# Optimization experiments

Hardware: AMD Instinct MI355X
Metric: run time of the kernel (lower is better)

Reference implementation:

```python
import jax, jax.numpy as jnp
import numpy as np

B, H, IN, OUT = 8192, 1024, 4, 4


def setup_inputs() -> dict:
    key = jax.random.key(0)
    ks = jax.random.split(key, 16)
    s = 1.0 / np.sqrt(H)

    def p(k, shape):
        return jax.random.uniform(k, shape, jnp.float32, -s, s)

    return {
        "context": jax.random.normal(ks[0], (B, H), jnp.float32),
        "wc": p(ks[1], (H // 2, H)),
        "bc": p(ks[2], (H // 2,)),
        "gru1_wi": p(ks[3], (3 * H, H // 2)),
        "gru1_wh": p(ks[4], (3 * H, H)),
        "gru1_bi": p(ks[5], (3 * H,)),
        "gru1_bh": p(ks[6], (3 * H,)),
        "gru2_wi": p(ks[7], (3 * H, H // 2)),
        "gru2_wh": p(ks[8], (3 * H, H)),
        "gru2_bi": p(ks[9], (3 * H,)),
        "gru2_bh": p(ks[10], (3 * H,)),
        "fc_in_w": p(ks[11], (IN, H)),
        "fc_in_b": p(ks[12], (IN,)),
        "fc_out_w": p(ks[13], (OUT, H)),
        "fc_out_b": p(ks[14], (OUT,)),
        "future_length": 30,
        "past_length": 60,
    }


def _gru_unroll(ec, h0, wi, wh, bi, bh, length):
    """Run a PyTorch-semantics GRUCell `length` steps with constant input ec.

    Returns all hidden states stacked: [T, B, H].
    """
    # Input-side gates are constant across steps (input is always ec).
    gi = ec @ wi.T + bi                     # [B, 3H]
    i_r, i_z, i_n = jnp.split(gi, 3, axis=-1)

    def step(h, _):
        gh = h @ wh.T + bh                  # [B, 3H]
        h_r, h_z, h_n = jnp.split(gh, 3, axis=-1)
        r = jax.nn.sigmoid(i_r + h_r)
        z = jax.nn.sigmoid(i_z + h_z)
        n = jnp.tanh(i_n + r * h_n)
        h_new = (1.0 - z) * n + z * h
        return h_new, h_new

    _, hs = jax.lax.scan(step, h0, None, length=length)
    return hs  # [T, B, H]


def reference(context, wc, bc,
              gru1_wi, gru1_wh, gru1_bi, gru1_bh,
              gru2_wi, gru2_wh, gru2_bi, gru2_bh,
              fc_in_w, fc_in_b, fc_out_w, fc_out_b,
              future_length, past_length):
    # encoded_context = relu(context_encoder(context))
    ec = jax.nn.relu(context @ wc.T + bc)   # [B, H/2]

    # Training-mode past-reconstruction branch (decoder1 + fc_in).
    hs1 = _gru_unroll(ec, context, gru1_wi, gru1_wh, gru1_bi, gru1_bh, past_length)
    decoded_inputs = jnp.einsum('tbh,ih->bti', hs1, fc_in_w) + fc_in_b  # [B, T_past, IN]

    # Future-prediction branch (decoder2 + relu + fc_out).
    hs2 = _gru_unroll(ec, context, gru2_wi, gru2_wh, gru2_bi, gru2_bh, future_length)
    outputs = jnp.einsum('tbh,oh->bto', jax.nn.relu(hs2), fc_out_w) + fc_out_b  # [B, T_fut, OUT]

    return (decoded_inputs, outputs)
```

## Files before the change

kernel.cpp:

```cpp
#include <hip/hip_runtime.h>
#include <math.h>

typedef __bf16 bf16;
typedef __bf16 bf16x8 __attribute__((ext_vector_type(8)));
typedef float f32x4 __attribute__((ext_vector_type(4)));

#define B_DIM 8192
#define H_DIM 1024
#define T_PAST 60
#define T_FUT 30

static __device__ __forceinline__ float sigm(float x) {
  return 1.f / (1.f + __expf(-x));
}
static __device__ __forceinline__ float tanh_fast(float x) {
  float xc = fminf(fmaxf(x, -10.f), 10.f);
  float e = __expf(2.f * xc);
  return (e - 1.f) / (e + 1.f);
}

__global__ void detect_dtype(const unsigned int* __restrict__ words,
                             int* __restrict__ is_bf16) {
  const int lane = threadIdx.x;
  int cnt = 0;
  for (int i = 0; i < 64; i++) {
    const unsigned int w = words[lane + i * 64];
    const int e = (w >> 7) & 0xFF;
    cnt += (e >= 100 && e <= 135) ? 1 : 0;
  }
  for (int off = 32; off > 0; off >>= 1) cnt += __shfl_down(cnt, off);
  if (lane == 0) *is_bf16 = (cnt >= 2048) ? 1 : 0;
}

struct ConvDesc { const void* src; bf16* dst; int n; };
struct ConvPack { ConvDesc d[15]; };

__global__ __launch_bounds__(256) void convert_all(ConvPack p,
                                                   const int* __restrict__ flag,
                                                   float* __restrict__ h0a,
                                                   float* __restrict__ h0b) {
  const int ti = blockIdx.y;
  const ConvDesc d = p.d[ti];
  const int bf = *flag;
  const long stride = (long)gridDim.x * 256 * 8;
  for (long base = ((long)blockIdx.x * 256 + threadIdx.x) * 8; base < d.n;
       base += stride) {
    if (base + 8 <= d.n) {
      float f[8];
      if (bf) {
        const uint4 v = *(const uint4*)((const char*)d.src + base * 2);
        *(uint4*)((char*)d.dst + base * 2) = v;
        if (ti == 0 && h0a) {
          const bf16* bv = (const bf16*)&v;
#pragma unroll
          for (int e = 0; e < 8; e++) f[e] = (float)bv[e];
        }
      } else {
        const float* s = (const float*)d.src + base;
        const float4 v0 = *(const float4*)s;
        const float4 v1 = *(const float4*)(s + 4);
        f[0] = v0.x; f[1] = v0.y; f[2] = v0.z; f[3] = v0.w;
        f[4] = v1.x; f[5] = v1.y; f[6] = v1.z; f[7] = v1.w;
        bf16 o[8];
#pragma unroll
        for (int e = 0; e < 8; e++) o[e] = (bf16)f[e];
        *(uint4*)((char*)d.dst + base * 2) = *(const uint4*)o;
      }
      if (ti == 0 && h0a) {
#pragma unroll
        for (int e = 0; e < 8; e++) { h0a[base + e] = f[e]; h0b[base + e] = f[e]; }
      }
    } else {
      for (long e = base; e < d.n; e++) {
        const float f = bf ? (float)((const bf16*)d.src)[e]
                           : ((const float*)d.src)[e];
        d.dst[e] = (bf16)f;
        if (ti == 0 && h0a) { h0a[e] = f; h0b[e] = f; }
      }
    }
  }
}

template <bool RELU, bool GI_BIAS>
__global__ __launch_bounds__(256, 2) void gemm_bt(
    const bf16* __restrict__ A, const bf16* __restrict__ Bm,
    const bf16* __restrict__ bias1, const bf16* __restrict__ bias2,
    bf16* __restrict__ C, int K, int N)
{
  __shared__ __attribute__((aligned(16))) bf16 As[128 * 32];
  __shared__ __attribute__((aligned(16))) bf16 Bs[128 * 32];
  const int tid = threadIdx.x;
  const int wave = tid >> 6, lane = tid & 63;
  const int quad = lane >> 4, l16 = lane & 15;
  const int m0 = blockIdx.x * 128, n0 = blockIdx.y * 128;
  const int wm = (wave & 1) * 64, wn = (wave >> 1) * 64;
  f32x4 acc[4][4] = {};
  for (int k0 = 0; k0 < K; k0 += 32) {
    bf16x8 va[2], vb[2];
#pragma unroll
    for (int rr = 0; rr < 2; rr++) {
      const int c = rr * 256 + tid;
      va[rr] = *(const bf16x8*)(A + (size_t)(m0 + (c >> 2)) * K + (k0 + (c & 3) * 8));
      vb[rr] = *(const bf16x8*)(Bm + (size_t)(n0 + (c >> 2)) * K + (k0 + (c & 3) * 8));
    }
#pragma unroll
    for (int rr = 0; rr < 2; rr++) {
      const int c = rr * 256 + tid;
      *(bf16x8*)(As + (c >> 2) * 32 + (c & 3) * 8) = va[rr];
      *(bf16x8*)(Bs + (c >> 2) * 32 + (c & 3) * 8) = vb[rr];
    }
    __syncthreads();
    bf16x8 af[4], bv[4];
#pragma unroll
    for (int t = 0; t < 4; t++) {
      af[t] = *(const bf16x8*)(As + ((wm + t * 16 + l16) * 32 + quad * 8));
      bv[t] = *(const bf16x8*)(Bs + ((wn + t * 16 + l16) * 32 + quad * 8));
    }
#pragma unroll
    for (int tm = 0; tm < 4; tm++)
#pragma unroll
      for (int tn = 0; tn < 4; tn++)
        acc[tm][tn] = __builtin_amdgcn_mfma_f32_16x16x32_bf16(af[tm], bv[tn], acc[tm][tn], 0, 0, 0);
    __syncthreads();
  }
#pragma unroll
  for (int tn = 0; tn < 4; tn++) {
    const int col = n0 + wn + tn * 16 + l16;
    float bias = (float)bias1[col];
    if (GI_BIAS) {
      if (col < 2 * H_DIM) bias += (float)bias2[col];
    }
#pragma unroll
    for (int tm = 0; tm < 4; tm++) {
#pragma unroll
      for (int r = 0; r < 4; r++) {
        const int row = m0 + wm + tm * 16 + quad * 4 + r;
        float v = acc[tm][tn][r] + bias;
        if (RELU) v = fmaxf(v, 0.f);
        C[(size_t)row * N + col] = (bf16)v;
      }
    }
  }
}

struct GruArgs {
  const bf16* h_in16; const float* h_in32;
  bf16* h_out16; float* h_out32;
  const bf16* gi;
  const bf16* wh;
  const bf16* bh;
  const bf16* fcw;
  float* proj;
  int projT, t, relu;
};

__global__ __launch_bounds__(256, 2) void gru_step(GruArgs g1, GruArgs g2)
{
  const GruArgs G = (blockIdx.z == 0) ? g1 : g2;
  __shared__ __attribute__((aligned(16))) bf16 As[128 * 32];
  __shared__ __attribute__((aligned(16))) bf16 Bs[192 * 32];
  const int tid = threadIdx.x;
  const int wave = tid >> 6, lane = tid & 63;
  const int quad = lane >> 4, l16 = lane & 15;
  const int m0 = blockIdx.x * 128;
  const int j0 = blockIdx.y * 64;
  f32x4 acc[2][12] = {};
  for (int k0 = 0; k0 < H_DIM; k0 += 32) {
    bf16x8 va[2], vb[3];
#pragma unroll
    for (int rr = 0; rr < 2; rr++) {
      const int c = rr * 256 + tid;
      va[rr] = *(const bf16x8*)(G.h_in16 + (size_t)(m0 + (c >> 2)) * H_DIM + (k0 + (c & 3) * 8));
    }
#pragma unroll
    for (int rr = 0; rr < 3; rr++) {
      const int c = rr * 256 + tid;
      const int p = c >> 2;
      const int grow = (p >> 6) * H_DIM + j0 + (p & 63);
      vb[rr] = *(const bf16x8*)(G.wh + (size_t)grow * H_DIM + (k0 + (c & 3) * 8));
    }
#pragma unroll
    for (int rr = 0; rr < 2; rr++) {
      const int c = rr * 256 + tid;
      *(bf16x8*)(As + (c >> 2) * 32 + (c & 3) * 8) = va[rr];
    }
#pragma unroll
    for (int rr = 0; rr < 3; rr++) {
      const int c = rr * 256 + tid;
      *(bf16x8*)(Bs + (c >> 2) * 32 + (c & 3) * 8) = vb[rr];
    }
    __syncthreads();
    bf16x8 af[2];
#pragma unroll
    for (int tm = 0; tm < 2; tm++)
      af[tm] = *(const bf16x8*)(As + ((wave * 32 + tm * 16 + l16) * 32 + quad * 8));
#pragma unroll
    for (int tn = 0; tn < 12; tn++) {
      bf16x8 bv = *(const bf16x8*)(Bs + ((tn * 16 + l16) * 32 + quad * 8));
      acc[0][tn] = __builtin_amdgcn_mfma_f32_16x16x32_bf16(af[0], bv, acc[0][tn], 0, 0, 0);
      acc[1][tn] = __builtin_amdgcn_mfma_f32_16x16x32_bf16(af[1], bv, acc[1][tn], 0, 0, 0);
    }
    __syncthreads();
  }
  float pp[2][4][4];
#pragma unroll
  for (int tm = 0; tm < 2; tm++)
#pragma unroll
    for (int r = 0; r < 4; r++)
#pragma unroll
      for (int i = 0; i < 4; i++) pp[tm][r][i] = 0.f;

#pragma unroll
  for (int tj = 0; tj < 4; tj++) {
    const int jj = tj * 16 + l16;
    const int j = j0 + jj;
    const float bhn = (float)G.bh[2 * H_DIM + j];
    float fw[4];
#pragma unroll
    for (int i = 0; i < 4; i++) fw[i] = (float)G.fcw[i * H_DIM + j];
#pragma unroll
    for (int tm = 0; tm < 2; tm++) {
#pragma unroll
      for (int r = 0; r < 4; r++) {
        const int row = m0 + wave * 32 + tm * 16 + quad * 4 + r;
        const size_t gb = (size_t)row * (3 * H_DIM) + j;
        const float gr = (float)G.gi[gb];
        const float gz = (float)G.gi[gb + H_DIM];
        const float gn = (float)G.gi[gb + 2 * H_DIM];
        const float hr = acc[tm][tj][r];
        const float hz = acc[tm][tj + 4][r];
        const float hn = acc[tm][tj + 8][r];
        const float rg = sigm(gr + hr);
        const float zg = sigm(gz + hz);
        const float ng = tanh_fast(gn + rg * (hn + bhn));
        const size_t hidx = (size_t)row * H_DIM + j;
        const float hold = G.h_in32 ? G.h_in32[hidx] : (float)G.h_in16[hidx];
        const float hnew = (1.f - zg) * ng + zg * hold;
        if (G.h_out32) G.h_out32[hidx] = hnew;
        G.h_out16[hidx] = (bf16)hnew;
        const float act = G.relu ? fmaxf(hnew, 0.f) : hnew;
#pragma unroll
        for (int i = 0; i < 4; i++) pp[tm][r][i] += fw[i] * act;
      }
    }
  }
#pragma unroll
  for (int tm = 0; tm < 2; tm++)
#pragma unroll
    for (int r = 0; r < 4; r++)
#pragma unroll
      for (int i = 0; i < 4; i++) {
        float v = pp[tm][r][i];
        v += __shfl_xor(v, 1);
        v += __shfl_xor(v, 2);
        v += __shfl_xor(v, 4);
        v += __shfl_xor(v, 8);
        if (l16 == 0) {
          const int row = m0 + wave * 32 + tm * 16 + quad * 4 + r;
          atomicAdd(&G.proj[((size_t)row * G.projT + G.t) * 4 + i], v);
        }
      }
}

__global__ __launch_bounds__(256) void finalize(const float* __restrict__ p1,
                                                const float* __restrict__ p2,
                                                const bf16* __restrict__ fib,
                                                const bf16* __restrict__ fob,
                                                const int* __restrict__ flag,
                                                void* __restrict__ out, int n) {
  const int idx = blockIdx.x * 256 + threadIdx.x;
  if (idx >= n) return;
  const int R1 = B_DIM * T_PAST * 4;
  float v;
  if (idx < R1) {
    v = p1[idx] + (float)fib[idx & 3];
  } else {
    const int k = idx - R1;
    v = p2[k] + (float)fob[k & 3];
  }
  if (*flag) ((bf16*)out)[idx] = (bf16)v;
  else       ((float*)out)[idx] = v;
}

extern "C" void kernel_launch(void* const* d_in, const int* in_sizes, int n_in,
                              void* d_out, int out_size, void* d_ws, size_t ws_size,
                              hipStream_t stream)
{
  (void)n_in;
  char* w = (char*)d_ws;
  auto alloc = [&](size_t bytes) -> void* {
    void* p = (void*)w;
    w += (bytes + 255) & ~(size_t)255;
    return p;
  };
  int* flag = (int*)alloc(256);

  bf16* canon[15];
  for (int i = 0; i < 15; i++) canon[i] = (bf16*)alloc((size_t)in_sizes[i] * 2);
  const bf16* ctx  = canon[0];
  const bf16* wc   = canon[1];
  const bf16* bc   = canon[2];
  const bf16* g1wi = canon[3];
  const bf16* g1wh = canon[4];
  const bf16* g1bi = canon[5];
  const bf16* g1bh = canon[6];
  const bf16* g2wi = canon[7];
  const bf16* g2wh = canon[8];
  const bf16* g2bi = canon[9];
  const bf16* g2bh = canon[10];
  const bf16* fiw  = canon[11];
  const bf16* fib  = canon[12];
  const bf16* fow  = canon[13];
  const bf16* fob  = canon[14];

  bf16* ec   = (bf16*)alloc((size_t)B_DIM * 512 * 2);
  bf16* gi1  = (bf16*)alloc((size_t)B_DIM * 3 * H_DIM * 2);
  bf16* gi2  = (bf16*)alloc((size_t)B_DIM * 3 * H_DIM * 2);
  bf16* h116[2] = {(bf16*)alloc((size_t)B_DIM * H_DIM * 2), (bf16*)alloc((size_t)B_DIM * H_DIM * 2)};
  bf16* h216[2] = {(bf16*)alloc((size_t)B_DIM * H_DIM * 2), (bf16*)alloc((size_t)B_DIM * H_DIM * 2)};
  float* proj1 = (float*)alloc((size_t)B_DIM * T_PAST * 4 * 4);
  float* proj2 = (float*)alloc((size_t)B_DIM * T_FUT * 4 * 4);
  float* h132[2] = {nullptr, nullptr};
  float* h232[2] = {nullptr, nullptr};
  const size_t used = (size_t)(w - (char*)d_ws);
  const size_t fp32_need = (size_t)4 * B_DIM * H_DIM * 4 + 4096;
  const bool fp32h = (ws_size > used) && ((ws_size - used) >= fp32_need);
  if (fp32h) {
    h132[0] = (float*)alloc((size_t)B_DIM * H_DIM * 4);
    h132[1] = (float*)alloc((size_t)B_DIM * H_DIM * 4);
    h232[0] = (float*)alloc((size_t)B_DIM * H_DIM * 4);
    h232[1] = (float*)alloc((size_t)B_DIM * H_DIM * 4);
  }

  detect_dtype<<<1, 64, 0, stream>>>((const unsigned int*)d_in[0], flag);

  hipMemsetAsync(proj1, 0,
                 ((size_t)B_DIM * T_PAST * 4 + (size_t)B_DIM * T_FUT * 4) * 4, stream);

  ConvPack cp;
  for (int i = 0; i < 15; i++) { cp.d[i].src = d_in[i]; cp.d[i].dst = canon[i]; cp.d[i].n = in_sizes[i]; }
  convert_all<<<dim3(4096, 15), 256, 0, stream>>>(cp, flag,
      fp32h ? h132[0] : nullptr, fp32h ? h232[0] : nullptr);

  gemm_bt<true, false><<<dim3(64, 4), 256, 0, stream>>>(ctx, wc, bc, nullptr, ec, H_DIM, 512);
  gemm_bt<false, true><<<dim3(64, 24), 256, 0, stream>>>(ec, g1wi, g1bi, g1bh, gi1, 512, 3 * H_DIM);
  gemm_bt<false, true><<<dim3(64, 24), 256, 0, stream>>>(ec, g2wi, g2bi, g2bh, gi2, 512, 3 * H_DIM);

  for (int t = 0; t < T_PAST; t++) {
    const int si = t & 1, so = (t + 1) & 1;
    GruArgs a1;
    a1.h_in16 = (t == 0) ? ctx : h116[si];
    a1.h_in32 = fp32h ? h132[si] : nullptr;
    a1.h_out16 = h116[so];
    a1.h_out32 = fp32h ? h132[so] : nullptr;
    a1.gi = gi1; a1.wh = g1wh; a1.bh = g1bh; a1.fcw = fiw;
    a1.proj = proj1; a1.projT = T_PAST; a1.t = t; a1.relu = 0;
    if (t < T_FUT) {
      GruArgs a2;
      a2.h_in16 = (t == 0) ? ctx : h216[si];
      a2.h_in32 = fp32h ? h232[si] : nullptr;
      a2.h_out16 = h216[so];
      a2.h_out32 = fp32h ? h232[so] : nullptr;
      a2.gi = gi2; a2.wh = g2wh; a2.bh = g2bh; a2.fcw = fow;
      a2.proj = proj2; a2.projT = T_FUT; a2.t = t; a2.relu = 1;
      gru_step<<<dim3(64, 16, 2), 256, 0, stream>>>(a1, a2);
    } else {
      gru_step<<<dim3(64, 16, 1), 256, 0, stream>>>(a1, a1);
    }
  }

  finalize<<<dim3((out_size + 255) / 256), 256, 0, stream>>>(
      proj1, proj2, fib, fob, flag, d_out, out_size);
}
```

Measured before the change: 10.76 ms.

## Use direct global-to-LDS loads with XOR swizzle and XCD-aware block remap

Replaces the register-staged global loads plus LDS stores in both the GEMM and the GRU step kernels with global_load_lds direct-to-LDS 16-byte transfers. The LDS layout is XOR-swizzled per row so the MFMA fragment reads avoid bank conflicts. The GRU step kernel also remaps block indices so blocks on the same XCD share weight-column slices, aiming for better L2 reuse of Wh. This cuts VGPR pressure and LDS write instructions but relies on the wave-contiguous LDS destination layout matching the swizzled addressing.

```diff
diff --git a/kernel.cpp b/kernel.cpp
--- a/kernel.cpp
+++ b/kernel.cpp
@@ -9,6 +9,12 @@
 #define H_DIM 1024
 #define T_PAST 60
 #define T_FUT 30
+
+static __device__ __forceinline__ void gld_lds16(const void* g, void* l) {
+  __builtin_amdgcn_global_load_lds(
+      (const __attribute__((address_space(1))) void*)g,
+      (__attribute__((address_space(3))) void*)l, 16, 0, 0);
+}
 
 static __device__ __forceinline__ float sigm(float x) {
   return 1.f / (1.f + __expf(-x));
@@ -96,25 +102,23 @@
   const int wm = (wave & 1) * 64, wn = (wave >> 1) * 64;
   f32x4 acc[4][4] = {};
   for (int k0 = 0; k0 < K; k0 += 32) {
-    bf16x8 va[2], vb[2];
 #pragma unroll
     for (int rr = 0; rr < 2; rr++) {
       const int c = rr * 256 + tid;
-      va[rr] = *(const bf16x8*)(A + (size_t)(m0 + (c >> 2)) * K + (k0 + (c & 3) * 8));
-      vb[rr] = *(const bf16x8*)(Bm + (size_t)(n0 + (c >> 2)) * K + (k0 + (c & 3) * 8));
-    }
-#pragma unroll
-    for (int rr = 0; rr < 2; rr++) {
-      const int c = rr * 256 + tid;
-      *(bf16x8*)(As + (c >> 2) * 32 + (c & 3) * 8) = va[rr];
-      *(bf16x8*)(Bs + (c >> 2) * 32 + (c & 3) * 8) = vb[rr];
+      const int cg = (c & 3) ^ ((c >> 3) & 3);
+      gld_lds16(A + (size_t)(m0 + (c >> 2)) * K + (k0 + cg * 8),
+                As + (size_t)(rr * 256 + wave * 64) * 8);
+      gld_lds16(Bm + (size_t)(n0 + (c >> 2)) * K + (k0 + cg * 8),
+                Bs + (size_t)(rr * 256 + wave * 64) * 8);
     }
     __syncthreads();
     bf16x8 af[4], bv[4];
 #pragma unroll
     for (int t = 0; t < 4; t++) {
-      af[t] = *(const bf16x8*)(As + ((wm + t * 16 + l16) * 32 + quad * 8));
-      bv[t] = *(const bf16x8*)(Bs + ((wn + t * 16 + l16) * 32 + quad * 8));
+      const int ra = wm + t * 16 + l16;
+      const int rb = wn + t * 16 + l16;
+      af[t] = *(const bf16x8*)(As + (ra * 32 + (quad ^ ((ra >> 1) & 3)) * 8));
+      bv[t] = *(const bf16x8*)(Bs + (rb * 32 + (quad ^ ((rb >> 1) & 3)) * 8));
     }
 #pragma unroll
     for (int tm = 0; tm < 4; tm++)
@@ -162,41 +166,39 @@
   const int tid = threadIdx.x;
   const int wave = tid >> 6, lane = tid & 63;
   const int quad = lane >> 4, l16 = lane & 15;
-  const int m0 = blockIdx.x * 128;
-  const int j0 = blockIdx.y * 64;
+  const int l = blockIdx.y * 64 + blockIdx.x;
+  const int xcd = l & 7, idx = l >> 3;
+  const int m0 = (idx & 63) * 128;
+  const int j0 = (xcd * 2 + (idx >> 6)) * 64;
   f32x4 acc[2][12] = {};
   for (int k0 = 0; k0 < H_DIM; k0 += 32) {
-    bf16x8 va[2], vb[3];
 #pragma unroll
     for (int rr = 0; rr < 2; rr++) {
       const int c = rr * 256 + tid;
-      va[rr] = *(const bf16x8*)(G.h_in16 + (size_t)(m0 + (c >> 2)) * H_DIM + (k0 + (c & 3) * 8));
+      const int cg = (c & 3) ^ ((c >> 3) & 3);
+      gld_lds16(G.h_in16 + (size_t)(m0 + (c >> 2)) * H_DIM + (k0 + cg * 8),
+                As + (size_t)(rr * 256 + wave * 64) * 8);
     }
 #pragma unroll
     for (int rr = 0; rr < 3; rr++) {
       const int c = rr * 256 + tid;
       const int p = c >> 2;
+      const int cg = (c & 3) ^ ((c >> 3) & 3);
       const int grow = (p >> 6) * H_DIM + j0 + (p & 63);
-      vb[rr] = *(const bf16x8*)(G.wh + (size_t)grow * H_DIM + (k0 + (c & 3) * 8));
-    }
-#pragma unroll
-    for (int rr = 0; rr < 2; rr++) {
-      const int c = rr * 256 + tid;
-      *(bf16x8*)(As + (c >> 2) * 32 + (c & 3) * 8) = va[rr];
-    }
-#pragma unroll
-    for (int rr = 0; rr < 3; rr++) {
-      const int c = rr * 256 + tid;
-      *(bf16x8*)(Bs + (c >> 2) * 32 + (c & 3) * 8) = vb[rr];
+      gld_lds16(G.wh + (size_t)grow * H_DIM + (k0 + cg * 8),
+                Bs + (size_t)(rr * 256 + wave * 64) * 8);
     }
     __syncthreads();
     bf16x8 af[2];
 #pragma unroll
-    for (int tm = 0; tm < 2; tm++)
-      af[tm] = *(const bf16x8*)(As + ((wave * 32 + tm * 16 + l16) * 32 + quad * 8));
+    for (int tm = 0; tm < 2; tm++) {
+      const int ra = wave * 32 + tm * 16 + l16;
+      af[tm] = *(const bf16x8*)(As + (ra * 32 + (quad ^ ((ra >> 1) & 3)) * 8));
+    }
 #pragma unroll
     for (int tn = 0; tn < 12; tn++) {
-      bf16x8 bv = *(const bf16x8*)(Bs + ((tn * 16 + l16) * 32 + quad * 8));
+      const int rb = tn * 16 + l16;
+      bf16x8 bv = *(const bf16x8*)(Bs + (rb * 32 + (quad ^ ((rb >> 1) & 3)) * 8));
       acc[0][tn] = __builtin_amdgcn_mfma_f32_16x16x32_bf16(af[0], bv, acc[0][tn], 0, 0, 0);
       acc[1][tn] = __builtin_amdgcn_mfma_f32_16x16x32_bf16(af[1], bv, acc[1][tn], 0, 0, 0);
     }
```

New measurement: 10.76 ms. About the same (-0.1%).
